# Optimization experiments

Hardware: AMD Instinct MI355X
Metric: run time of the kernel (lower is better)

Reference implementation:

```python
import math
import jax, jax.numpy as jnp
import numpy as np

B, T, E = 4, 2048, 768
H, D = 3, E // 3  # 3 heads, head_dim = emb_sz // 3
USE_MASK = True


def setup_inputs() -> dict:
    key = jax.random.key(0)
    ks = jax.random.split(key, 8)
    s_in = 1.0 / math.sqrt(E)
    return {
        "inputs_for_keys": jax.random.normal(ks[0], (B, T, E), jnp.float32),
        "inputs_for_values": jax.random.normal(ks[1], (B, T, E), jnp.float32),
        "inputs_for_queries": jax.random.normal(ks[2], (B, T, E), jnp.float32),
        # per-head projection weights, stacked over head axis: [H, E, D]
        "Wk": jax.random.normal(ks[3], (H, E, D), jnp.float32) * s_in,
        "Wq": jax.random.normal(ks[4], (H, E, D), jnp.float32) * s_in,
        "Wv": jax.random.normal(ks[5], (H, E, D), jnp.float32) * s_in,
        # final Dense(emb_sz)
        "Wo": jax.random.normal(ks[6], (E, E), jnp.float32) * s_in,
        "bo": jnp.zeros((E,), jnp.float32),
    }


def reference(inputs_for_keys, inputs_for_values, inputs_for_queries, Wk, Wq, Wv, Wo, bo):
    # Project per head: [B,T,E] x [H,E,D] -> [B,H,T,D]
    K = jnp.einsum('bte,hed->bhtd', inputs_for_keys, Wk)
    V = jnp.einsum('bte,hed->bhtd', inputs_for_values, Wv)
    Q = jnp.einsum('bte,hed->bhtd', inputs_for_queries, Wq)
    # NOTE: original scales by sqrt(window_size_keys) = sqrt(T), not sqrt(D)
    scores = jnp.einsum('bhqd,bhkd->bhqk', Q, K) / math.sqrt(T)
    if USE_MASK:
        mask = jnp.triu(jnp.full((T, T), -jnp.inf, dtype=scores.dtype), k=1)
        scores = scores + mask
    attn = jax.nn.softmax(scores, axis=-1)  # [B,H,Tq,Tk]
    z = jnp.einsum('bhqk,bhkd->bhqd', attn, V)  # [B,H,T,D]
    # concat heads in order head1,head2,head3 along last axis -> [B,T,E]
    z = jnp.transpose(z, (0, 2, 1, 3)).reshape(B, T, H * D)
    return z @ Wo + bo
```

## Files before the change

kernel.cpp:

```cpp
#include <hip/hip_runtime.h>
#include <hip/hip_bf16.h>
#include <math.h>

#define B_ 4
#define T_ 2048
#define E_ 768
#define H_ 3
#define D_ 256
#define LOG2E 1.4426950408889634f

typedef __attribute__((ext_vector_type(8))) _Float16 half8;
typedef __attribute__((ext_vector_type(8))) unsigned short ushort8;
typedef __attribute__((ext_vector_type(4))) float f32x4;

static __device__ inline unsigned short f2h(float x) {
    _Float16 h = (_Float16)x;
    return *reinterpret_cast<unsigned short*>(&h);
}

#define GLOAD_LDS(SRC, DST) \
    __builtin_amdgcn_global_load_lds( \
        (const __attribute__((address_space(1))) void*)(SRC), \
        (__attribute__((address_space(3))) void*)(DST), 16, 0, 0)

__global__ __launch_bounds__(256)
void transpose_cast_all(const float* __restrict__ Wk, const float* __restrict__ Wq,
                        const float* __restrict__ Wv, const float* __restrict__ Wo,
                        unsigned short* __restrict__ WTk, unsigned short* __restrict__ WTq,
                        unsigned short* __restrict__ WTv, unsigned short* __restrict__ WoT)
{
    __shared__ float tile[32][33];
    const int z = blockIdx.z;
    const float* in; unsigned short* out; int R, C;
    if (z < 9) {
        const int mat = z / 3, hd = z % 3;
        R = E_; C = D_;
        in  = (mat == 0 ? Wk  : mat == 1 ? Wq  : Wv)  + (long)hd * E_ * D_;
        out = (mat == 0 ? WTk : mat == 1 ? WTq : WTv) + (long)hd * D_ * E_;
    } else {
        R = E_; C = E_;
        in = Wo; out = WoT;
    }
    const int c0 = blockIdx.x * 32;
    const int r0 = blockIdx.y * 32;
    if (c0 >= C) return;
    const int t  = threadIdx.x;
    const int cc = t & 31, rr = t >> 5;
    #pragma unroll
    for (int i = 0; i < 4; ++i)
        tile[rr + i * 8][cc] = in[(long)(r0 + rr + i * 8) * C + c0 + cc];
    __syncthreads();
    const int rr2 = t & 31, cc2 = t >> 5;
    #pragma unroll
    for (int i = 0; i < 4; ++i)
        out[(long)(c0 + cc2 + i * 8) * R + r0 + rr2] = f2h(tile[rr2][cc2 + i * 8]);
}

__global__ __launch_bounds__(256)
void transpose16(const unsigned short* __restrict__ in, unsigned short* __restrict__ out,
                 int R, int Ccols)
{
    __shared__ unsigned short tile[64 * 64];
    char* tb = (char*)tile;
    const long zoff = (long)blockIdx.z * R * Ccols;
    const int r0 = blockIdx.y * 64, c0 = blockIdx.x * 64;
    const int t = threadIdx.x;
    #pragma unroll
    for (int i = 0; i < 2; ++i) {
        const int rr = (t >> 3) + i * 32;
        const int gc = (t & 7) * 8;
        ushort8 v = *(const ushort8*)(in + zoff + (long)(r0 + rr) * Ccols + c0 + gc);
        *(ushort8*)(tb + rr * 128 + ((gc * 2) ^ (((rr >> 3) & 7) << 4))) = v;
    }
    __syncthreads();
    #pragma unroll
    for (int i = 0; i < 2; ++i) {
        const int cc = (t >> 3) + i * 32;
        const int gr = (t & 7) * 8;
        ushort8 v;
        #pragma unroll
        for (int e = 0; e < 8; ++e) {
            const int row = gr + e;
            v[e] = *(const unsigned short*)(tb + row * 128 + ((cc * 2) ^ (((row >> 3) & 7) << 4)));
        }
        *(ushort8*)(out + zoff + (long)(c0 + cc) * R + r0 + gr) = v;
    }
}

template<bool CONVA, bool OUT16>
__device__ __forceinline__
void gemm_body(const float* Af, const unsigned short* Ah, const unsigned short* Bz,
               void* Cz, const float* bias, int K, int lda, int ldc,
               int m0, int n0, int tid)
{
    __shared__ unsigned short As[128 * 32];
    __shared__ unsigned short Bs[128 * 32];

    const int lane = tid & 63, wid = tid >> 6;
    const int wm = wid >> 1, wn = wid & 1;
    const int fr = lane & 15, fg = lane >> 4;

    f32x4 acc[4][4];
    #pragma unroll
    for (int mt = 0; mt < 4; ++mt)
        #pragma unroll
        for (int nt = 0; nt < 4; ++nt) acc[mt][nt] = (f32x4)(0.f);

    for (int k0 = 0; k0 < K; k0 += 32) {
        #pragma unroll
        for (int i = 0; i < 2; ++i) {
            const int G = tid + i * 256;
            const int row = G >> 2, g = G & 3;
            ushort8 pa;
            if (CONVA) {
                const float* s = Af + (long)(m0 + row) * lda + k0 + g * 8;
                float4 f0 = *(const float4*)s, f1 = *(const float4*)(s + 4);
                pa[0] = f2h(f0.x); pa[1] = f2h(f0.y); pa[2] = f2h(f0.z); pa[3] = f2h(f0.w);
                pa[4] = f2h(f1.x); pa[5] = f2h(f1.y); pa[6] = f2h(f1.z); pa[7] = f2h(f1.w);
            } else {
                pa = *(const ushort8*)(Ah + (long)(m0 + row) * lda + k0 + g * 8);
            }
            *(ushort8*)&As[row * 32 + g * 8] = pa;
            *(ushort8*)&Bs[row * 32 + g * 8] =
                *(const ushort8*)(Bz + (long)(n0 + row) * K + k0 + g * 8);
        }
        __syncthreads();

        half8 a[4], b[4];
        #pragma unroll
        for (int mt = 0; mt < 4; ++mt)
            a[mt] = *(const half8*)&As[(wm * 64 + mt * 16 + fr) * 32 + fg * 8];
        #pragma unroll
        for (int nt = 0; nt < 4; ++nt)
            b[nt] = *(const half8*)&Bs[(wn * 64 + nt * 16 + fr) * 32 + fg * 8];
        #pragma unroll
        for (int mt = 0; mt < 4; ++mt)
            #pragma unroll
            for (int nt = 0; nt < 4; ++nt)
                acc[mt][nt] = __builtin_amdgcn_mfma_f32_16x16x32_f16(
                                  a[mt], b[nt], acc[mt][nt], 0, 0, 0);
        __syncthreads();
    }

    #pragma unroll
    for (int nt = 0; nt < 4; ++nt) {
        const int col = n0 + wn * 64 + nt * 16 + fr;
        const float badd = bias ? bias[col] : 0.f;
        #pragma unroll
        for (int mt = 0; mt < 4; ++mt) {
            const int row = m0 + wm * 64 + mt * 16 + fg * 4;
            #pragma unroll
            for (int reg = 0; reg < 4; ++reg) {
                if (OUT16)
                    ((unsigned short*)Cz)[(long)(row + reg) * ldc + col] =
                        f2h(acc[mt][nt][reg] + badd);
                else
                    ((float*)Cz)[(long)(row + reg) * ldc + col] =
                        acc[mt][nt][reg] + badd;
            }
        }
    }
}

template<bool CONVA, bool OUT16>
__global__ __launch_bounds__(256)
void gemm_mfma(const void* __restrict__ Av, const unsigned short* __restrict__ Bt,
               void* __restrict__ Cv, const float* __restrict__ bias,
               int K, int Hdiv, int lda, int ldc, long sA, long sB, long sC)
{
    const int z = blockIdx.z;
    const float*          Af = (const float*)Av          + (long)(z / Hdiv) * sA;
    const unsigned short* Ah = (const unsigned short*)Av + (long)(z / Hdiv) * sA;
    const unsigned short* Bz = Bt + (long)(z % Hdiv) * sB;
    void* Cz = OUT16 ? (void*)((unsigned short*)Cv + (long)z * sC)
                     : (void*)((float*)Cv + (long)z * sC);
    gemm_body<CONVA, OUT16>(Af, Ah, Bz, Cz, bias, K, lda, ldc,
                            blockIdx.y * 128, blockIdx.x * 128, threadIdx.x);
}

__global__ __launch_bounds__(256)
void qkv_proj(const float* __restrict__ Xk, const float* __restrict__ Xv,
              const float* __restrict__ Xq,
              const unsigned short* __restrict__ WTk, const unsigned short* __restrict__ WTv,
              const unsigned short* __restrict__ WTq,
              unsigned short* __restrict__ Kp, unsigned short* __restrict__ Vp,
              unsigned short* __restrict__ Qp)
{
    const int z = blockIdx.z;
    const int which = z / 12, bh = z % 12;
    const int b = bh / H_, h = bh % H_;
    const float* X = (which == 0) ? Xk : (which == 1) ? Xv : Xq;
    const unsigned short* W = (which == 0) ? WTk : (which == 1) ? WTv : WTq;
    unsigned short* P = (which == 0) ? Kp : (which == 1) ? Vp : Qp;
    const float* Af = X + (long)b * T_ * E_;
    const unsigned short* Bz = W + (long)h * D_ * E_;
    unsigned short* Cz = P + (long)bh * T_ * D_;
    gemm_body<true, true>(Af, nullptr, Bz, Cz, nullptr, E_, E_, D_,
                          blockIdx.y * 128, blockIdx.x * 128, threadIdx.x);
}

__global__ __launch_bounds__(256, 2)
void flash_lds(const unsigned short* __restrict__ Qb, const unsigned short* __restrict__ Kb,
               const unsigned short* __restrict__ Vtb, unsigned short* __restrict__ Z2h,
               float scale_log2e)
{
    __shared__ unsigned short Ktile[2][32 * 256];
    __shared__ unsigned short Vtile[2][256 * 32];
    __shared__ unsigned short Ps[4][16 * 72];

    const int p  = blockIdx.x;
    const int bh = p % 12;
    const int pi = p / 12;
    const int qtB = 63 - pi;
    const int b = bh / H_, h = bh % H_;
    const int tid = threadIdx.x;
    const int w = tid >> 6, lane = tid & 63;
    const int g = lane >> 4, fr = lane & 15;
    const int qw0 = (w < 2) ? (pi * 32 + w * 16) : (qtB * 32 + (w - 2) * 16);

    const unsigned short* kg = Kb  + (long)bh * T_ * D_;
    const unsigned short* vg = Vtb + (long)bh * D_ * T_;

    const unsigned short* qrow = Qb + ((long)bh * T_ + qw0 + fr) * D_;
    const _Float16 hs = (_Float16)scale_log2e;
    half8 qf[8];
    #pragma unroll
    for (int c = 0; c < 8; ++c) {
        qf[c] = *(const half8*)(qrow + c * 32 + g * 8);
        qf[c] *= hs;
    }

    f32x4 o[16];
    #pragma unroll
    for (int dt = 0; dt < 16; ++dt) o[dt] = (f32x4)(0.f);
    float mrow[4] = {-INFINITY, -INFINITY, -INFINITY, -INFINITY};
    float lrow[4] = {0.f, 0.f, 0.f, 0.f};

    const int nkt = qtB + 1;

    auto STAGE = [&](int bufi, int kt) {
        const int k0 = kt * 32;
        #pragma unroll
        for (int i = 0; i < 4; ++i) {
            const int L = tid + i * 256;
            const int r = L >> 5, cg = L & 31;
            GLOAD_LDS(kg + (long)(k0 + r) * D_ + ((cg ^ (r & 7)) * 8),
                      &Ktile[bufi][L * 8]);
        }
        #pragma unroll
        for (int i = 0; i < 4; ++i) {
            const int L = tid + i * 256;
            const int dr = L >> 2, gq = L & 3;
            GLOAD_LDS(vg + (long)dr * T_ + k0 + ((gq ^ ((dr >> 1) & 3)) * 8),
                      &Vtile[bufi][L * 8]);
        }
    };

    STAGE(0, 0);
    int buf = 0;
    for (int kt = 0; kt < nkt; ++kt) {
        asm volatile("s_waitcnt vmcnt(0)" ::: "memory");
        __builtin_amdgcn_sched_barrier(0);
        __builtin_amdgcn_s_barrier();
        __builtin_amdgcn_sched_barrier(0);
        if (kt + 1 < nkt)
            STAGE(buf ^ 1, kt + 1);

        const int k0 = kt * 32;
        if (k0 <= qw0 + 15) {
            f32x4 s[2];
            s[0] = (f32x4)(0.f); s[1] = (f32x4)(0.f);
            const int kkey = fr & 7;
            __builtin_amdgcn_s_setprio(1);
            #pragma unroll
            for (int c = 0; c < 8; ++c) {
                #pragma unroll
                for (int nt = 0; nt < 2; ++nt) {
                    const int kr = nt * 16 + fr;
                    half8 kf = *(const half8*)&Ktile[buf][(kr * 32 + ((c * 4 + g) ^ kkey)) * 8];
                    s[nt] = __builtin_amdgcn_mfma_f32_16x16x32_f16(qf[c], kf, s[nt], 0, 0, 0);
                }
            }
            __builtin_amdgcn_s_setprio(0);

            const bool diag = (k0 + 31 > qw0);
            float sv[2][4];
            #pragma unroll
            for (int nt = 0; nt < 2; ++nt)
                #pragma unroll
                for (int reg = 0; reg < 4; ++reg) {
                    float v = s[nt][reg];
                    if (diag && (k0 + nt * 16 + fr > qw0 + g * 4 + reg)) v = -INFINITY;
                    sv[nt][reg] = v;
                }

            float pmax[4];
            #pragma unroll
            for (int reg = 0; reg < 4; ++reg) pmax[reg] = fmaxf(sv[0][reg], sv[1][reg]);
            const bool ok = (pmax[0] <= mrow[0] + 8.f) && (pmax[1] <= mrow[1] + 8.f)
                         && (pmax[2] <= mrow[2] + 8.f) && (pmax[3] <= mrow[3] + 8.f);
            if (!__all(ok)) {
                #pragma unroll
                for (int reg = 0; reg < 4; ++reg) {
                    float tm = pmax[reg];
                    tm = fmaxf(tm, __shfl_xor(tm, 1));
                    tm = fmaxf(tm, __shfl_xor(tm, 2));
                    tm = fmaxf(tm, __shfl_xor(tm, 4));
                    tm = fmaxf(tm, __shfl_xor(tm, 8));
                    const float mnew = fmaxf(mrow[reg], tm);
                    const float alpha = exp2f(mrow[reg] - mnew);
                    mrow[reg] = mnew;
                    lrow[reg] *= alpha;
                    #pragma unroll
                    for (int dt = 0; dt < 16; ++dt) o[dt][reg] *= alpha;
                }
            }
            #pragma unroll
            for (int nt = 0; nt < 2; ++nt)
                #pragma unroll
                for (int reg = 0; reg < 4; ++reg) {
                    const float pp = exp2f(sv[nt][reg] - mrow[reg]);
                    lrow[reg] += pp;
                    Ps[w][(g * 4 + reg) * 72 + nt * 16 + fr] = f2h(pp);
                }

            const half8 pf0 = *(const half8*)&Ps[w][fr * 72 + g * 8];

            const int vkey = g ^ ((fr >> 1) & 3);
            __builtin_amdgcn_s_setprio(1);
            #pragma unroll
            for (int dt = 0; dt < 16; ++dt) {
                const int dr = dt * 16 + fr;
                half8 vf = *(const half8*)&Vtile[buf][(dr * 4 + vkey) * 8];
                o[dt] = __builtin_amdgcn_mfma_f32_16x16x32_f16(pf0, vf, o[dt], 0, 0, 0);
            }
            __builtin_amdgcn_s_setprio(0);
        }
        buf ^= 1;
    }

    float inv[4];
    #pragma unroll
    for (int reg = 0; reg < 4; ++reg) {
        float ps = lrow[reg];
        ps += __shfl_xor(ps, 1);
        ps += __shfl_xor(ps, 2);
        ps += __shfl_xor(ps, 4);
        ps += __shfl_xor(ps, 8);
        inv[reg] = 1.f / ps;
    }
    const long rowbase = ((long)b * T_ + qw0 + g * 4) * E_ + h * D_;
    #pragma unroll
    for (int reg = 0; reg < 4; ++reg) {
        unsigned short* dst = Z2h + rowbase + (long)reg * E_ + fr;
        #pragma unroll
        for (int dt = 0; dt < 16; ++dt)
            dst[dt * 16] = f2h(o[dt][reg] * inv[reg]);
    }
}

extern "C" void kernel_launch(void* const* d_in, const int* in_sizes, int n_in,
                              void* d_out, int out_size, void* d_ws, size_t ws_size,
                              hipStream_t stream)
{
    const float* Xk = (const float*)d_in[0];
    const float* Xv = (const float*)d_in[1];
    const float* Xq = (const float*)d_in[2];
    const float* Wk = (const float*)d_in[3];
    const float* Wq = (const float*)d_in[4];
    const float* Wv = (const float*)d_in[5];
    const float* Wo = (const float*)d_in[6];
    const float* bo = (const float*)d_in[7];
    float* out = (float*)d_out;

    const size_t phd = (size_t)B_ * H_ * T_ * D_;
    const size_t wsz = (size_t)H_ * E_ * D_;
    unsigned short* Kp  = (unsigned short*)d_ws;
    unsigned short* Vp  = Kp + phd;
    unsigned short* Qp  = Vp + phd;
    unsigned short* Vt  = Qp + phd;
    unsigned short* Z2h = Vt + phd;
    unsigned short* WTk = Z2h + (size_t)B_ * T_ * E_;
    unsigned short* WTq = WTk + wsz;
    unsigned short* WTv = WTq + wsz;
    unsigned short* WoT = WTv + wsz;

    dim3 blk(256);

    dim3 gtw(E_ / 32, E_ / 32, 10);
    transpose_cast_all<<<gtw, blk, 0, stream>>>(Wk, Wq, Wv, Wo, WTk, WTq, WTv, WoT);

    dim3 gproj(D_ / 128, T_ / 128, 36);
    qkv_proj<<<gproj, blk, 0, stream>>>(Xk, Xv, Xq, WTk, WTv, WTq, Kp, Vp, Qp);

    dim3 gtv(D_ / 64, T_ / 64, B_ * H_);
    transpose16<<<gtv, blk, 0, stream>>>(Vp, Vt, T_, D_);

    dim3 gf(32 * B_ * H_);
    flash_lds<<<gf, blk, 0, stream>>>(Qp, Kp, Vt, Z2h,
                                      0.022097086912079608f * LOG2E);

    dim3 gout(E_ / 128, (B_ * T_) / 128, 1);
    gemm_mfma<false, false><<<gout, blk, 0, stream>>>(Z2h, WoT, out, bo, E_, 1, E_, E_,
                                                      0L, 0L, 0L);
}
```

Measured before the change: 202.0 us.

## Write V projection transposed directly and remap flash-attention block order

The V projection GEMM now writes its output in transposed [D,T] layout from the epilogue, so the separate transpose16 kernel and its round trip through global memory are removed. The flash attention kernel also gets a new block-index mapping that interleaves (b,h) pairs across XCD-style strides of 8 and pairs short and long causal query tiles in alternating order, to balance load and improve cache locality. The transposed epilogue writes are strided scalar 16-bit stores, which may coalesce poorly.

```diff
diff --git a/kernel.cpp b/kernel.cpp
--- a/kernel.cpp
+++ b/kernel.cpp
@@ -56,38 +56,7 @@
         out[(long)(c0 + cc2 + i * 8) * R + r0 + rr2] = f2h(tile[rr2][cc2 + i * 8]);
 }
 
-__global__ __launch_bounds__(256)
-void transpose16(const unsigned short* __restrict__ in, unsigned short* __restrict__ out,
-                 int R, int Ccols)
-{
-    __shared__ unsigned short tile[64 * 64];
-    char* tb = (char*)tile;
-    const long zoff = (long)blockIdx.z * R * Ccols;
-    const int r0 = blockIdx.y * 64, c0 = blockIdx.x * 64;
-    const int t = threadIdx.x;
-    #pragma unroll
-    for (int i = 0; i < 2; ++i) {
-        const int rr = (t >> 3) + i * 32;
-        const int gc = (t & 7) * 8;
-        ushort8 v = *(const ushort8*)(in + zoff + (long)(r0 + rr) * Ccols + c0 + gc);
-        *(ushort8*)(tb + rr * 128 + ((gc * 2) ^ (((rr >> 3) & 7) << 4))) = v;
-    }
-    __syncthreads();
-    #pragma unroll
-    for (int i = 0; i < 2; ++i) {
-        const int cc = (t >> 3) + i * 32;
-        const int gr = (t & 7) * 8;
-        ushort8 v;
-        #pragma unroll
-        for (int e = 0; e < 8; ++e) {
-            const int row = gr + e;
-            v[e] = *(const unsigned short*)(tb + row * 128 + ((cc * 2) ^ (((row >> 3) & 7) << 4)));
-        }
-        *(ushort8*)(out + zoff + (long)(c0 + cc) * R + r0 + gr) = v;
-    }
-}
-
-template<bool CONVA, bool OUT16>
+template<bool CONVA, bool OUT16, bool TRANSC>
 __device__ __forceinline__
 void gemm_body(const float* Af, const unsigned short* Ah, const unsigned short* Bz,
                void* Cz, const float* bias, int K, int lda, int ldc,
@@ -151,12 +120,13 @@
             const int row = m0 + wm * 64 + mt * 16 + fg * 4;
             #pragma unroll
             for (int reg = 0; reg < 4; ++reg) {
-                if (OUT16)
-                    ((unsigned short*)Cz)[(long)(row + reg) * ldc + col] =
-                        f2h(acc[mt][nt][reg] + badd);
+                const float vv = acc[mt][nt][reg] + badd;
+                if (TRANSC)
+                    ((unsigned short*)Cz)[(long)col * ldc + row + reg] = f2h(vv);
+                else if (OUT16)
+                    ((unsigned short*)Cz)[(long)(row + reg) * ldc + col] = f2h(vv);
                 else
-                    ((float*)Cz)[(long)(row + reg) * ldc + col] =
-                        acc[mt][nt][reg] + badd;
+                    ((float*)Cz)[(long)(row + reg) * ldc + col] = vv;
             }
         }
     }
@@ -174,8 +144,8 @@
     const unsigned short* Bz = Bt + (long)(z % Hdiv) * sB;
     void* Cz = OUT16 ? (void*)((unsigned short*)Cv + (long)z * sC)
                      : (void*)((float*)Cv + (long)z * sC);
-    gemm_body<CONVA, OUT16>(Af, Ah, Bz, Cz, bias, K, lda, ldc,
-                            blockIdx.y * 128, blockIdx.x * 128, threadIdx.x);
+    gemm_body<CONVA, OUT16, false>(Af, Ah, Bz, Cz, bias, K, lda, ldc,
+                                   blockIdx.y * 128, blockIdx.x * 128, threadIdx.x);
 }
 
 __global__ __launch_bounds__(256)
@@ -183,20 +153,28 @@
               const float* __restrict__ Xq,
               const unsigned short* __restrict__ WTk, const unsigned short* __restrict__ WTv,
               const unsigned short* __restrict__ WTq,
-              unsigned short* __restrict__ Kp, unsigned short* __restrict__ Vp,
+              unsigned short* __restrict__ Kp, unsigned short* __restrict__ Vt,
               unsigned short* __restrict__ Qp)
 {
     const int z = blockIdx.z;
     const int which = z / 12, bh = z % 12;
     const int b = bh / H_, h = bh % H_;
-    const float* X = (which == 0) ? Xk : (which == 1) ? Xv : Xq;
-    const unsigned short* W = (which == 0) ? WTk : (which == 1) ? WTv : WTq;
-    unsigned short* P = (which == 0) ? Kp : (which == 1) ? Vp : Qp;
-    const float* Af = X + (long)b * T_ * E_;
-    const unsigned short* Bz = W + (long)h * D_ * E_;
-    unsigned short* Cz = P + (long)bh * T_ * D_;
-    gemm_body<true, true>(Af, nullptr, Bz, Cz, nullptr, E_, E_, D_,
-                          blockIdx.y * 128, blockIdx.x * 128, threadIdx.x);
+    const int m0 = blockIdx.y * 128, n0 = blockIdx.x * 128;
+    const int tid = threadIdx.x;
+    if (which == 1) {
+        const float* Af = Xv + (long)b * T_ * E_;
+        const unsigned short* Bz = WTv + (long)h * D_ * E_;
+        unsigned short* Cz = Vt + (long)bh * D_ * T_;
+        gemm_body<true, true, true>(Af, nullptr, Bz, Cz, nullptr, E_, E_, T_, m0, n0, tid);
+    } else {
+        const float* X = (which == 0) ? Xk : Xq;
+        const unsigned short* W = (which == 0) ? WTk : WTq;
+        unsigned short* P = (which == 0) ? Kp : Qp;
+        const float* Af = X + (long)b * T_ * E_;
+        const unsigned short* Bz = W + (long)h * D_ * E_;
+        unsigned short* Cz = P + (long)bh * T_ * D_;
+        gemm_body<true, true, false>(Af, nullptr, Bz, Cz, nullptr, E_, E_, D_, m0, n0, tid);
+    }
 }
 
 __global__ __launch_bounds__(256, 2)
@@ -209,8 +187,10 @@
     __shared__ unsigned short Ps[4][16 * 72];
 
     const int p  = blockIdx.x;
-    const int bh = p % 12;
-    const int pi = p / 12;
+    const int l  = (p & 7) * 48 + (p >> 3);
+    const int bh = l >> 5;
+    const int jj = l & 31;
+    const int pi = (jj & 1) ? (31 - (jj >> 1)) : (jj >> 1);
     const int qtB = 63 - pi;
     const int b = bh / H_, h = bh % H_;
     const int tid = threadIdx.x;
@@ -391,10 +371,7 @@
     transpose_cast_all<<<gtw, blk, 0, stream>>>(Wk, Wq, Wv, Wo, WTk, WTq, WTv, WoT);
 
     dim3 gproj(D_ / 128, T_ / 128, 36);
-    qkv_proj<<<gproj, blk, 0, stream>>>(Xk, Xv, Xq, WTk, WTv, WTq, Kp, Vp, Qp);
-
-    dim3 gtv(D_ / 64, T_ / 64, B_ * H_);
-    transpose16<<<gtv, blk, 0, stream>>>(Vp, Vt, T_, D_);
+    qkv_proj<<<gproj, blk, 0, stream>>>(Xk, Xv, Xq, WTk, WTv, WTq, Kp, Vt, Qp);
 
     dim3 gf(32 * B_ * H_);
     flash_lds<<<gf, blk, 0, stream>>>(Qp, Kp, Vt, Z2h,
```

Result: no change. 202.4 us (+0.2%).
